# Optimization experiments

Hardware: AMD Instinct MI355X
Metric: run time of the kernel (lower is better)

## Reference

```python
import jax, jax.numpy as jnp
import numpy as np

M_USERS = 100000
N_ITEMS = 50000
NUM_NODES = M_USERS + N_ITEMS
DIM = 64
N_EDGES = 3200000
BATCH = 1024
N_NEGS = 40
REG = 1e-4
NUM_LAYERS = 2


def setup_inputs() -> dict:
    key = jax.random.key(0)
    ks = jax.random.split(key, 14)
    xav = lambda k, shp: jax.random.normal(k, shp, dtype=jnp.float32) * np.float32(np.sqrt(2.0 / (shp[0] + shp[-1])))
    return {
        "E": xav(ks[0], (NUM_NODES, DIM)),
        "E2": xav(ks[1], (NUM_NODES, DIM)),
        "W0": xav(ks[2], (DIM, DIM)),
        "b0": jnp.zeros((DIM,), jnp.float32),
        "W1": xav(ks[3], (DIM, DIM)),
        "b1": jnp.zeros((DIM,), jnp.float32),
        "attn_W": xav(ks[4], (DIM, DIM)),
        "attn_b": jnp.zeros((DIM,), jnp.float32),
        "q_W": xav(ks[5], (1, DIM)),
        "w": jax.random.normal(ks[6], (BATCH,), dtype=jnp.float32),
        "edge_index": jax.random.randint(ks[7], (2, N_EDGES), 0, NUM_NODES, dtype=jnp.int64),
        "u": jax.random.randint(ks[8], (BATCH,), 0, M_USERS, dtype=jnp.int64),
        "v": jax.random.randint(ks[9], (BATCH,), 0, NUM_NODES, dtype=jnp.int64),
        "n": jax.random.randint(ks[10], (BATCH, N_NEGS), 0, NUM_NODES, dtype=jnp.int64),
    }


def _aggregate(E, E2, W0, b0, W1, b1, attn_W, attn_b, q_W, row, col):
    # LightGCN branch: symmetric degree-normalized scatter-add, NUM_LAYERS hops
    deg = jax.ops.segment_sum(jnp.ones_like(col, dtype=E.dtype), col, num_segments=NUM_NODES)
    dinv = jnp.where(deg > 0, jax.lax.rsqrt(jnp.maximum(deg, 1e-12)), 0.0)
    norm = dinv[row] * dinv[col]  # [E]

    def conv(x):
        msg = norm[:, None] * x[row]  # [E, D]
        return jax.ops.segment_sum(msg, col, num_segments=NUM_NODES)

    acc = E
    x = E
    for _ in range(NUM_LAYERS):
        x = conv(x)
        acc = acc + x
    z_p = acc / (NUM_LAYERS + 1)

    # MLP branch (eval mode: dropout disabled)
    h = jax.nn.relu(E2 @ W0.T + b0)
    z_n = jax.nn.relu(h @ W1.T + b1)

    # attention fusion
    w_p = jnp.tanh(z_p @ attn_W.T + attn_b) @ q_W.T  # [NUM_NODES, 1]
    w_n = jnp.tanh(z_n @ attn_W.T + attn_b) @ q_W.T
    alpha = jax.nn.softmax(jnp.concatenate([w_p, w_n], axis=1), axis=1)
    return alpha[:, :1] * z_p + alpha[:, 1:] * z_n


def reference(E, E2, W0, b0, W1, b1, attn_W, attn_b, q_W, w, edge_index, u, v, n):
    row, col = edge_index[0], edge_index[1]
    Z = _aggregate(E, E2, W0, b0, W1, b1, attn_W, attn_b, q_W, row, col)
    u_ = Z[u]            # [B, D]
    v_ = Z[v]            # [B, D]
    n_ = Z[n]            # [B, K, D]
    pos = jnp.sum(u_ * v_, axis=1)                      # [B]
    neg = jnp.einsum('bd,bkd->bk', u_, n_)              # [B, K]
    coef = -0.5 * jnp.sign(w) + 1.5                     # [B]
    sbpr = jax.nn.log_sigmoid(coef[:, None] * pos[:, None] - neg)  # [B, K]
    reg_loss = jnp.sum(u_ ** 2) + jnp.sum(v_ ** 2) + jnp.sum(n_ ** 2)
    return -jnp.sum(sbpr) + REG * reg_loss
```

## Files before the change

### kernel.cpp

```cpp
#include <hip/hip_runtime.h>
#include <hip/hip_fp8.h>
#include <math.h>

#define NUM_NODES 150000
#define DIM 64
#define N_EDGES 3200000
#define BATCH 1024
#define N_NEGS 40
#define REG_COEF 1e-4f

#define BK_BITS 9
#define BK_NODES 512
#define NBK ((NUM_NODES + BK_NODES - 1) >> BK_BITS)
#define TILE 8192
#define NT ((N_EDGES + TILE - 1) / TILE)
#define HSIZE (NBK * NT)
#define SCAN_B 1024
#define NB2 ((HSIZE + SCAN_B - 1) / SCAN_B)
#define NB3 ((NUM_NODES + SCAN_B - 1) / SCAN_B)
#define NLIST (BATCH * (N_NEGS + 2))

typedef _Float16 half2v __attribute__((ext_vector_type(2)));
typedef _Float16 half4v __attribute__((ext_vector_type(4)));

__global__ __launch_bounds__(256) void histo_kernel(const int* __restrict__ col,
                                                    int* __restrict__ hist) {
    __shared__ int h[NBK];
    int t = threadIdx.x;
    for (int i = t; i < NBK; i += 256) h[i] = 0;
    __syncthreads();
    int e0 = blockIdx.x * TILE;
    int e1 = e0 + TILE; if (e1 > N_EDGES) e1 = N_EDGES;
    for (int i = e0 + t; i < e1; i += 256) atomicAdd(&h[col[i] >> BK_BITS], 1);
    __syncthreads();
    for (int i = t; i < NBK; i += 256) hist[i * NT + blockIdx.x] = h[i];
}

__global__ void scan_partial_kernel(const int* __restrict__ src, int* __restrict__ partial, int n) {
    int t = threadIdx.x;
    int g = blockIdx.x * SCAN_B + t;
    int v = (g < n) ? src[g] : 0;
    for (int m = 1; m < 64; m <<= 1) v += __shfl_xor(v, m);
    __shared__ int ws[16];
    if ((t & 63) == 0) ws[t >> 6] = v;
    __syncthreads();
    if (t < 16) {
        int s = ws[t];
        for (int m = 1; m < 16; m <<= 1) s += __shfl_xor(s, m);
        if (t == 0) partial[blockIdx.x] = s;
    }
}

__global__ void scan_base_kernel(int* __restrict__ partial, int nb, int chunks) {
    int l = threadIdx.x;
    int carry = 0;
    for (int c = 0; c < chunks; c++) {
        int idx = c * 64 + l;
        int v = (idx < nb) ? partial[idx] : 0;
        int inc = v;
        for (int m = 1; m < 64; m <<= 1) {
            int t = __shfl_up(inc, m);
            if (l >= m) inc += t;
        }
        int excl = inc - v + carry;
        if (idx < nb) partial[idx] = excl;
        carry += __shfl(inc, 63);
    }
}

__global__ void scan_apply_kernel(int* __restrict__ data, const int* __restrict__ partial, int n) {
    __shared__ int lds[SCAN_B];
    int t = threadIdx.x;
    int g = blockIdx.x * SCAN_B + t;
    int v = (g < n) ? data[g] : 0;
    int val = v;
    lds[t] = val;
    __syncthreads();
    for (int o = 1; o < SCAN_B; o <<= 1) {
        int add = (t >= o) ? lds[t - o] : 0;
        __syncthreads();
        val += add;
        lds[t] = val;
        __syncthreads();
    }
    if (g < n) data[g] = partial[blockIdx.x] + val - v;
}

__global__ void scan_apply2_kernel(const int* __restrict__ src, int* __restrict__ dst,
                                   const int* __restrict__ partial, int n) {
    __shared__ int lds[SCAN_B];
    int t = threadIdx.x;
    int g = blockIdx.x * SCAN_B + t;
    int v = (g < n) ? src[g] : 0;
    int val = v;
    lds[t] = val;
    __syncthreads();
    for (int o = 1; o < SCAN_B; o <<= 1) {
        int add = (t >= o) ? lds[t - o] : 0;
        __syncthreads();
        val += add;
        lds[t] = val;
        __syncthreads();
    }
    if (g < n) dst[g] = partial[blockIdx.x] + val - v;
}

__global__ __launch_bounds__(256) void partition_kernel(const int* __restrict__ row,
                                                        const int* __restrict__ col,
                                                        const int* __restrict__ hist,
                                                        unsigned* __restrict__ staging) {
    __shared__ int base[NBK];
    __shared__ int cnt[NBK];
    int t = threadIdx.x;
    for (int i = t; i < NBK; i += 256) { base[i] = hist[i * NT + blockIdx.x]; cnt[i] = 0; }
    __syncthreads();
    int e0 = blockIdx.x * TILE;
    int e1 = e0 + TILE; if (e1 > N_EDGES) e1 = N_EDGES;
    for (int i = e0 + t; i < e1; i += 256) {
        int c = col[i];
        int b = c >> BK_BITS;
        int r = atomicAdd(&cnt[b], 1);
        staging[base[b] + r] = ((unsigned)(c & (BK_NODES - 1)) << 18) | (unsigned)row[i];
    }
}

__global__ __launch_bounds__(512) void fill3_kernel(const int* __restrict__ hist,
                                                    const unsigned* __restrict__ staging,
                                                    const float* __restrict__ E,
                                                    int* __restrict__ off,
                                                    float* __restrict__ dinv,
                                                    float* __restrict__ sq,
                                                    int* __restrict__ csr_row,
                                                    __hip_fp8x4_e4m3* __restrict__ xnE4) {
    __shared__ int cnt[BK_NODES];
    __shared__ int lds[BK_NODES];
    __shared__ float sdinv[BK_NODES];
    int b = blockIdx.x;
    int t = threadIdx.x;
    int node0 = b << BK_BITS;
    int bstart = hist[b * NT];
    int bend = (b + 1 < NBK) ? hist[(b + 1) * NT] : N_EDGES;
    cnt[t] = 0;
    __syncthreads();
    for (int i = bstart + t; i < bend; i += 512) atomicAdd(&cnt[staging[i] >> 18], 1);
    __syncthreads();
    int v = cnt[t];
    int val = v;
    lds[t] = val;
    __syncthreads();
    for (int o = 1; o < BK_NODES; o <<= 1) {
        int add = (t >= o) ? lds[t - o] : 0;
        __syncthreads();
        val += add;
        lds[t] = val;
        __syncthreads();
    }
    int cursor = bstart + val - v;
    int node = node0 + t;
    float dv = (v > 0) ? rsqrtf((float)v) : 0.f;
    if (node < NUM_NODES) {
        off[node] = cursor;
        dinv[node] = dv;
        sq[node] = sqrtf((float)v);
    }
    sdinv[t] = dv;
    cnt[t] = cursor;
    __syncthreads();
    for (int i = bstart + t; i < bend; i += 512) {
        unsigned s = staging[i];
        int pos = atomicAdd(&cnt[s >> 18], 1);
        csr_row[pos] = (int)(s & 0x3FFFFu);
    }
    int nvalid = NUM_NODES - node0; if (nvalid > BK_NODES) nvalid = BK_NODES;
    int groups = nvalid << 4;
    const float4* E4 = (const float4*)E + ((size_t)node0 << 4);
    __hip_fp8x4_e4m3* out4 = xnE4 + ((size_t)node0 << 4);
    for (int gi = t; gi < groups; gi += 512) {
        float4 e = E4[gi];
        float s = 16.f * sdinv[gi >> 4];
        out4[gi] = __hip_fp8x4_e4m3(make_float4(s * e.x, s * e.y, s * e.z, s * e.w));
    }
    if (b == 0 && t == 0) off[NUM_NODES] = N_EDGES;
}

__global__ void flag_kernel(const int* __restrict__ u, const int* __restrict__ v,
                            const int* __restrict__ n, int* __restrict__ flags) {
    int i = blockIdx.x * blockDim.x + threadIdx.x;
    if (i >= NLIST) return;
    int id;
    if (i < BATCH) id = u[i];
    else if (i < 2 * BATCH) id = v[i - BATCH];
    else id = n[i - 2 * BATCH];
    flags[id] = 1;
}

__global__ void emit_list_kernel(const int* __restrict__ flags, const int* __restrict__ posb,
                                 int* __restrict__ list, int* __restrict__ count) {
    int i = blockIdx.x * blockDim.x + threadIdx.x;
    if (i >= NUM_NODES) return;
    if (flags[i]) list[posb[i]] = i;
    if (i == NUM_NODES - 1) *count = posb[i] + flags[i];
}

__global__ __launch_bounds__(256) void conv1_kernel(const int* __restrict__ off,
                                                    const int* __restrict__ csr_row,
                                                    const float* __restrict__ dinv,
                                                    const __hip_fp8x4_e4m3* __restrict__ xq,
                                                    _Float16* __restrict__ yh) {
    int gid = blockIdx.x * blockDim.x + threadIdx.x;
    int grp = gid >> 4;
    int g = threadIdx.x & 15;
    if (grp >= NUM_NODES) return;
    int start = off[grp];
    int end = off[grp + 1];
    float a0 = 0.f, a1 = 0.f, a2 = 0.f, a3 = 0.f;
    int i = start;
    for (; i + 3 < end; i += 4) {
        int r0 = csr_row[i];
        int r1 = csr_row[i + 1];
        int r2 = csr_row[i + 2];
        int r3 = csr_row[i + 3];
        float4 v0 = static_cast<float4>(xq[((size_t)r0 << 4) + g]);
        float4 v1 = static_cast<float4>(xq[((size_t)r1 << 4) + g]);
        float4 v2 = static_cast<float4>(xq[((size_t)r2 << 4) + g]);
        float4 v3 = static_cast<float4>(xq[((size_t)r3 << 4) + g]);
        a0 += v0.x + v1.x + v2.x + v3.x;
        a1 += v0.y + v1.y + v2.y + v3.y;
        a2 += v0.z + v1.z + v2.z + v3.z;
        a3 += v0.w + v1.w + v2.w + v3.w;
    }
    for (; i < end; ++i) {
        int r = csr_row[i];
        float4 v = static_cast<float4>(xq[((size_t)r << 4) + g]);
        a0 += v.x; a1 += v.y; a2 += v.z; a3 += v.w;
    }
    float dv = dinv[grp];
    float s = dv * dv * (1.f / 16.f);
    union { _Float16 h[4]; short4 s4; } u;
    u.h[0] = (_Float16)(s * a0);
    u.h[1] = (_Float16)(s * a1);
    u.h[2] = (_Float16)(s * a2);
    u.h[3] = (_Float16)(s * a3);
    ((short4*)yh)[((size_t)grp << 4) + g] = u.s4;
}

__global__ __launch_bounds__(256) void conv2_kernel(const int* __restrict__ off,
                                                    const int* __restrict__ csr_row,
                                                    const float* __restrict__ dinv,
                                                    const _Float16* __restrict__ xh,
                                                    float* __restrict__ x2,
                                                    const int* __restrict__ list,
                                                    const int* __restrict__ count) {
    int gid = blockIdx.x * blockDim.x + threadIdx.x;
    int li = gid >> 4;
    int g = threadIdx.x & 15;
    if (li >= *count) return;
    int nd = list[li];
    int start = off[nd];
    int end = off[nd + 1];
    const short4* xh4 = (const short4*)xh;
    float a0 = 0.f, a1 = 0.f, a2 = 0.f, a3 = 0.f;
    int i = start;
    for (; i + 3 < end; i += 4) {
        int r0 = csr_row[i];
        int r1 = csr_row[i + 1];
        int r2 = csr_row[i + 2];
        int r3 = csr_row[i + 3];
        union { short4 s4; _Float16 h[4]; } u0, u1, u2, u3;
        u0.s4 = xh4[((size_t)r0 << 4) + g];
        u1.s4 = xh4[((size_t)r1 << 4) + g];
        u2.s4 = xh4[((size_t)r2 << 4) + g];
        u3.s4 = xh4[((size_t)r3 << 4) + g];
        a0 += (float)u0.h[0] + (float)u1.h[0] + (float)u2.h[0] + (float)u3.h[0];
        a1 += (float)u0.h[1] + (float)u1.h[1] + (float)u2.h[1] + (float)u3.h[1];
        a2 += (float)u0.h[2] + (float)u1.h[2] + (float)u2.h[2] + (float)u3.h[2];
        a3 += (float)u0.h[3] + (float)u1.h[3] + (float)u2.h[3] + (float)u3.h[3];
    }
    for (; i < end; ++i) {
        int r = csr_row[i];
        union { short4 s4; _Float16 h[4]; } u;
        u.s4 = xh4[((size_t)r << 4) + g];
        a0 += (float)u.h[0]; a1 += (float)u.h[1];
        a2 += (float)u.h[2]; a3 += (float)u.h[3];
    }
    float dv = dinv[nd];
    ((float4*)x2)[((size_t)nd << 4) + g] = make_float4(dv * a0, dv * a1, dv * a2, dv * a3);
}

__global__ __launch_bounds__(256, 4) void fuse_kernel(
    const float* __restrict__ E, const float* __restrict__ E2,
    const float* __restrict__ W0, const float* __restrict__ b0,
    const float* __restrict__ W1, const float* __restrict__ b1,
    const float* __restrict__ AW, const float* __restrict__ ab,
    const float* __restrict__ qW,
    const _Float16* __restrict__ xn1, const float* __restrict__ sq,
    const float* x2, float* Z,
    const int* __restrict__ list, const int* __restrict__ count) {
    __shared__ __align__(16) _Float16 W0h[4096];
    __shared__ __align__(16) _Float16 W1h[4096];
    __shared__ __align__(16) _Float16 AWh[4096];
    __shared__ float bb0[64], bb1[64], bab[64], qb[64];
    __shared__ __align__(16) _Float16 xb[4][64];
    __shared__ __align__(16) _Float16 hb[4][64];
    __shared__ __align__(16) _Float16 zpb[4][64];
    __shared__ __align__(16) _Float16 znb[4][64];

    int t = threadIdx.x;
    for (int idx = t; idx < 4096; idx += 256) {
        int j = idx >> 6, k = idx & 63;
        int dst = (k >> 2) * 256 + j * 4 + (k & 3);
        W0h[dst] = (_Float16)W0[idx];
        W1h[dst] = (_Float16)W1[idx];
        AWh[dst] = (_Float16)AW[idx];
    }
    if (t < 64) { bb0[t] = b0[t]; bb1[t] = b1[t]; bab[t] = ab[t]; qb[t] = qW[t]; }
    __syncthreads();

    const int lane = t & 63, w = t >> 6;
    const int cnt = *count;
    const int stride = gridDim.x * 4;
    int li = blockIdx.x * 4 + w;
    if (li >= cnt) return;

    int ndA = list[li];
    {
    }
    size_t bA0 = ((size_t)ndA << 6) + lane;
    float eA = E[bA0], e2A = E2[bA0], x2A = x2[bA0], sqA = sq[ndA];
    _Float16 xnA = xn1[bA0];

    for (; li < cnt; li += stride) {
        int liB = li + stride; liB = (liB < cnt) ? liB : (cnt - 1);
        int ndB = list[liB];
        size_t bB = ((size_t)ndB << 6) + lane;
        float eB = E[bB], e2B = E2[bB], x2B = x2[bB], sqB = sq[ndB];
        _Float16 xnB = xn1[bB];

        size_t base = ((size_t)ndA << 6) + lane;
        float x1v = sqA * (float)xnA;
        float zp = (eA + x1v + x2A) * (1.f / 3.f);
        zpb[w][lane] = (_Float16)zp;
        xb[w][lane] = (_Float16)e2A;
        __builtin_amdgcn_wave_barrier();

        float s0 = bb0[lane], s1 = 0.f;
#pragma unroll
        for (int k4 = 0; k4 < 16; k4++) {
            half4v w4 = *(const half4v*)&W0h[k4 * 256 + lane * 4];
            half4v x4 = *(const half4v*)&xb[w][k4 * 4];
            s0 = __builtin_amdgcn_fdot2((half2v){w4.x, w4.y}, (half2v){x4.x, x4.y}, s0, false);
            s1 = __builtin_amdgcn_fdot2((half2v){w4.z, w4.w}, (half2v){x4.z, x4.w}, s1, false);
        }
        float h = fmaxf(s0 + s1, 0.f);
        hb[w][lane] = (_Float16)h;
        __builtin_amdgcn_wave_barrier();

        s0 = bb1[lane]; s1 = 0.f;
#pragma unroll
        for (int k4 = 0; k4 < 16; k4++) {
            half4v w4 = *(const half4v*)&W1h[k4 * 256 + lane * 4];
            half4v x4 = *(const half4v*)&hb[w][k4 * 4];
            s0 = __builtin_amdgcn_fdot2((half2v){w4.x, w4.y}, (half2v){x4.x, x4.y}, s0, false);
            s1 = __builtin_amdgcn_fdot2((half2v){w4.z, w4.w}, (half2v){x4.z, x4.w}, s1, false);
        }
        float zn = fmaxf(s0 + s1, 0.f);
        znb[w][lane] = (_Float16)zn;
        __builtin_amdgcn_wave_barrier();

        float sp0 = bab[lane], sp1 = 0.f, sn0 = 0.f, sn1 = 0.f;
#pragma unroll
        for (int k4 = 0; k4 < 16; k4++) {
            half4v w4 = *(const half4v*)&AWh[k4 * 256 + lane * 4];
            half4v p4 = *(const half4v*)&zpb[w][k4 * 4];
            half4v n4 = *(const half4v*)&znb[w][k4 * 4];
            sp0 = __builtin_amdgcn_fdot2((half2v){w4.x, w4.y}, (half2v){p4.x, p4.y}, sp0, false);
            sp1 = __builtin_amdgcn_fdot2((half2v){w4.z, w4.w}, (half2v){p4.z, p4.w}, sp1, false);
            sn0 = __builtin_amdgcn_fdot2((half2v){w4.x, w4.y}, (half2v){n4.x, n4.y}, sn0, false);
            sn1 = __builtin_amdgcn_fdot2((half2v){w4.z, w4.w}, (half2v){n4.z, n4.w}, sn1, false);
        }
        float tp = tanhf(sp0 + sp1) * qb[lane];
        float tn = tanhf(bab[lane] + sn0 + sn1) * qb[lane];
        for (int m = 1; m < 64; m <<= 1) {
            tp += __shfl_xor(tp, m);
            tn += __shfl_xor(tn, m);
        }
        float mx = fmaxf(tp, tn);
        float ep = expf(tp - mx), en = expf(tn - mx);
        float inv = 1.f / (ep + en);
        Z[base] = (ep * zp + en * zn) * inv;
        __builtin_amdgcn_wave_barrier();

        ndA = ndB; eA = eB; e2A = e2B; xnA = xnB; x2A = x2B; sqA = sqB;
    }
}

__global__ __launch_bounds__(256) void loss_kernel(const float* __restrict__ Z,
                                                   const float* __restrict__ wv,
                                                   const int* __restrict__ u,
                                                   const int* __restrict__ v,
                                                   const int* __restrict__ n,
                                                   float* __restrict__ out) {
    int wid = (blockIdx.x * blockDim.x + threadIdx.x) >> 6;
    int lane = threadIdx.x & 63;
    if (wid >= BATCH) return;
    float uu = Z[(size_t)u[wid] * DIM + lane];
    float vv = Z[(size_t)v[wid] * DIM + lane];
    float pos = uu * vv;
    for (int m = 1; m < 64; m <<= 1) pos += __shfl_xor(pos, m);
    float reg = uu * uu + vv * vv;
    float wval = wv[wid];
    float sgn = (wval > 0.f ? 1.f : 0.f) - (wval < 0.f ? 1.f : 0.f);
    float coef = -0.5f * sgn + 1.5f;
    float cp = coef * pos;
    float sb = 0.f;
    for (int k = 0; k < N_NEGS; k++) {
        int nid = n[wid * N_NEGS + k];
        float nn = Z[(size_t)nid * DIM + lane];
        float d = uu * nn;
        for (int m = 1; m < 64; m <<= 1) d += __shfl_xor(d, m);
        reg += nn * nn;
        float x = cp - d;
        float ls = (x >= 0.f) ? -log1pf(expf(-x)) : (x - log1pf(expf(x)));
        sb += ls;
    }
    for (int m = 1; m < 64; m <<= 1) reg += __shfl_xor(reg, m);
    if (lane == 0) atomicAdd(out, -sb + REG_COEF * reg);
}

extern "C" void kernel_launch(void* const* d_in, const int* in_sizes, int n_in,
                              void* d_out, int out_size, void* d_ws, size_t ws_size,
                              hipStream_t stream) {
    const float* E  = (const float*)d_in[0];
    const float* E2 = (const float*)d_in[1];
    const float* W0 = (const float*)d_in[2];
    const float* b0 = (const float*)d_in[3];
    const float* W1 = (const float*)d_in[4];
    const float* b1 = (const float*)d_in[5];
    const float* AW = (const float*)d_in[6];
    const float* ab = (const float*)d_in[7];
    const float* qW = (const float*)d_in[8];
    const float* wv = (const float*)d_in[9];
    const int* ei   = (const int*)d_in[10];
    const int* uu   = (const int*)d_in[11];
    const int* vv   = (const int*)d_in[12];
    const int* nn   = (const int*)d_in[13];
    const int* row = ei;
    const int* col = ei + N_EDGES;

    char* ws = (char*)d_ws;
    size_t p = 0;
    auto align_up = [](size_t x) { return (x + 255) & ~(size_t)255; };
    int* off        = (int*)(ws + p); p = align_up(p + (size_t)(NUM_NODES + 1) * 4);
    float* dinv     = (float*)(ws + p); p = align_up(p + (size_t)NUM_NODES * 4);
    float* sq       = (float*)(ws + p); p = align_up(p + (size_t)NUM_NODES * 4);
    int* hist       = (int*)(ws + p); p = align_up(p + (size_t)HSIZE * 4);
    int* partial    = (int*)(ws + p); p = align_up(p + (size_t)NB2 * 4);
    int* csr_row    = (int*)(ws + p); p = align_up(p + (size_t)N_EDGES * 4);
    int* flagi      = (int*)(ws + p); p = align_up(p + (size_t)NUM_NODES * 4);
    int* posb       = (int*)(ws + p); p = align_up(p + (size_t)NUM_NODES * 4);
    int* list       = (int*)(ws + p); p = align_up(p + (size_t)NLIST * 4);
    int* count      = (int*)(ws + p); p = align_up(p + 4);
    __hip_fp8x4_e4m3* xnE4 = (__hip_fp8x4_e4m3*)(ws + p); p = align_up(p + (size_t)NUM_NODES * DIM);
    _Float16* xn1   = (_Float16*)(ws + p); p = align_up(p + (size_t)NUM_NODES * DIM * 2);
    float* x2f      = (float*)(ws + p); p = align_up(p + (size_t)NUM_NODES * DIM * 4);
    float* Z = x2f;
    unsigned* staging = (unsigned*)x2f;

    hipMemsetAsync(d_out, 0, sizeof(float), stream);
    hipMemsetAsync(flagi, 0, (size_t)NUM_NODES * 4, stream);

    histo_kernel<<<NT, 256, 0, stream>>>(col, hist);
    scan_partial_kernel<<<NB2, SCAN_B, 0, stream>>>(hist, partial, HSIZE);
    scan_base_kernel<<<1, 64, 0, stream>>>(partial, NB2, 2);
    scan_apply_kernel<<<NB2, SCAN_B, 0, stream>>>(hist, partial, HSIZE);
    partition_kernel<<<NT, 256, 0, stream>>>(row, col, hist, staging);
    fill3_kernel<<<NBK, 512, 0, stream>>>(hist, staging, E, off, dinv, sq, csr_row, xnE4);

    flag_kernel<<<(NLIST + 255) / 256, 256, 0, stream>>>(uu, vv, nn, flagi);
    scan_partial_kernel<<<NB3, SCAN_B, 0, stream>>>(flagi, partial, NUM_NODES);
    scan_base_kernel<<<1, 64, 0, stream>>>(partial, NB3, 3);
    scan_apply2_kernel<<<NB3, SCAN_B, 0, stream>>>(flagi, posb, partial, NUM_NODES);
    emit_list_kernel<<<(NUM_NODES + 255) / 256, 256, 0, stream>>>(flagi, posb, list, count);

    conv1_kernel<<<(NUM_NODES * 16 + 255) / 256, 256, 0, stream>>>(off, csr_row, dinv, xnE4, xn1);
    conv2_kernel<<<(NLIST * 16 + 255) / 256, 256, 0, stream>>>(off, csr_row, dinv, xn1, x2f, list, count);

    fuse_kernel<<<1280, 256, 0, stream>>>(E, E2, W0, b0, W1, b1, AW, ab, qW,
                                          xn1, sq, x2f, Z, list, count);

    loss_kernel<<<BATCH * 64 / 256, 256, 0, stream>>>(Z, wv, uu, vv, nn, (float*)d_out);
}
```

Measured before the change: 270.5 us.

## Keep fuse weights in registers, process four nodes per wave, unroll conv1 by eight

The fuse kernel now holds each lane's rows of W0, W1 and attn_W as fp16 pairs in registers instead of staging them in shared memory. Each wave now handles a chunk of four nodes per iteration, so every weight register is reused across four dot products and the next chunk's inputs are prefetched. This raises register pressure, so occupancy is lowered to launch_bounds(256,2). Separately, conv1's gather loop is unrolled from four to eight edges to keep more independent loads in flight.

```diff
diff --git a/kernel.cpp b/kernel.cpp
--- a/kernel.cpp
+++ b/kernel.cpp
@@ -215,19 +215,17 @@
     int end = off[grp + 1];
     float a0 = 0.f, a1 = 0.f, a2 = 0.f, a3 = 0.f;
     int i = start;
-    for (; i + 3 < end; i += 4) {
-        int r0 = csr_row[i];
-        int r1 = csr_row[i + 1];
-        int r2 = csr_row[i + 2];
-        int r3 = csr_row[i + 3];
-        float4 v0 = static_cast<float4>(xq[((size_t)r0 << 4) + g]);
-        float4 v1 = static_cast<float4>(xq[((size_t)r1 << 4) + g]);
-        float4 v2 = static_cast<float4>(xq[((size_t)r2 << 4) + g]);
-        float4 v3 = static_cast<float4>(xq[((size_t)r3 << 4) + g]);
-        a0 += v0.x + v1.x + v2.x + v3.x;
-        a1 += v0.y + v1.y + v2.y + v3.y;
-        a2 += v0.z + v1.z + v2.z + v3.z;
-        a3 += v0.w + v1.w + v2.w + v3.w;
+    for (; i + 7 < end; i += 8) {
+        int r[8];
+#pragma unroll
+        for (int k = 0; k < 8; k++) r[k] = csr_row[i + k];
+        float4 v[8];
+#pragma unroll
+        for (int k = 0; k < 8; k++) v[k] = static_cast<float4>(xq[((size_t)r[k] << 4) + g]);
+#pragma unroll
+        for (int k = 0; k < 8; k++) {
+            a0 += v[k].x; a1 += v[k].y; a2 += v[k].z; a3 += v[k].w;
+        }
     }
     for (; i < end; ++i) {
         int r = csr_row[i];
@@ -287,7 +285,7 @@
     ((float4*)x2)[((size_t)nd << 4) + g] = make_float4(dv * a0, dv * a1, dv * a2, dv * a3);
 }
 
-__global__ __launch_bounds__(256, 4) void fuse_kernel(
+__global__ __launch_bounds__(256, 2) void fuse_kernel(
     const float* __restrict__ E, const float* __restrict__ E2,
     const float* __restrict__ W0, const float* __restrict__ b0,
     const float* __restrict__ W1, const float* __restrict__ b1,
@@ -296,101 +294,136 @@
     const _Float16* __restrict__ xn1, const float* __restrict__ sq,
     const float* x2, float* Z,
     const int* __restrict__ list, const int* __restrict__ count) {
-    __shared__ __align__(16) _Float16 W0h[4096];
-    __shared__ __align__(16) _Float16 W1h[4096];
-    __shared__ __align__(16) _Float16 AWh[4096];
-    __shared__ float bb0[64], bb1[64], bab[64], qb[64];
-    __shared__ __align__(16) _Float16 xb[4][64];
-    __shared__ __align__(16) _Float16 hb[4][64];
-    __shared__ __align__(16) _Float16 zpb[4][64];
-    __shared__ __align__(16) _Float16 znb[4][64];
-
-    int t = threadIdx.x;
-    for (int idx = t; idx < 4096; idx += 256) {
-        int j = idx >> 6, k = idx & 63;
-        int dst = (k >> 2) * 256 + j * 4 + (k & 3);
-        W0h[dst] = (_Float16)W0[idx];
-        W1h[dst] = (_Float16)W1[idx];
-        AWh[dst] = (_Float16)AW[idx];
-    }
-    if (t < 64) { bb0[t] = b0[t]; bb1[t] = b1[t]; bab[t] = ab[t]; qb[t] = qW[t]; }
-    __syncthreads();
-
+    const int t = threadIdx.x;
     const int lane = t & 63, w = t >> 6;
+
+    half2v w0r[32], w1r[32], awr[32];
+    {
+        const float4* W0v = (const float4*)(W0 + lane * 64);
+        const float4* W1v = (const float4*)(W1 + lane * 64);
+        const float4* AWv = (const float4*)(AW + lane * 64);
+#pragma unroll
+        for (int k = 0; k < 16; k++) {
+            float4 a = W0v[k];
+            w0r[2 * k] = (half2v){(_Float16)a.x, (_Float16)a.y};
+            w0r[2 * k + 1] = (half2v){(_Float16)a.z, (_Float16)a.w};
+            float4 b = W1v[k];
+            w1r[2 * k] = (half2v){(_Float16)b.x, (_Float16)b.y};
+            w1r[2 * k + 1] = (half2v){(_Float16)b.z, (_Float16)b.w};
+            float4 c = AWv[k];
+            awr[2 * k] = (half2v){(_Float16)c.x, (_Float16)c.y};
+            awr[2 * k + 1] = (half2v){(_Float16)c.z, (_Float16)c.w};
+        }
+    }
+    const float bb0 = b0[lane], bb1 = b1[lane], bab = ab[lane], qb = qW[lane];
+
+    __shared__ __align__(16) _Float16 xb[4][4][64];
+    __shared__ __align__(16) _Float16 zpb[4][4][64];
+    __shared__ __align__(16) _Float16 hb[4][4][64];
+    __shared__ __align__(16) _Float16 znb[4][4][64];
+
     const int cnt = *count;
-    const int stride = gridDim.x * 4;
-    int li = blockIdx.x * 4 + w;
-    if (li >= cnt) return;
-
-    int ndA = list[li];
-    {
-    }
-    size_t bA0 = ((size_t)ndA << 6) + lane;
-    float eA = E[bA0], e2A = E2[bA0], x2A = x2[bA0], sqA = sq[ndA];
-    _Float16 xnA = xn1[bA0];
-
-    for (; li < cnt; li += stride) {
-        int liB = li + stride; liB = (liB < cnt) ? liB : (cnt - 1);
-        int ndB = list[liB];
-        size_t bB = ((size_t)ndB << 6) + lane;
-        float eB = E[bB], e2B = E2[bB], x2B = x2[bB], sqB = sq[ndB];
-        _Float16 xnB = xn1[bB];
-
-        size_t base = ((size_t)ndA << 6) + lane;
-        float x1v = sqA * (float)xnA;
-        float zp = (eA + x1v + x2A) * (1.f / 3.f);
-        zpb[w][lane] = (_Float16)zp;
-        xb[w][lane] = (_Float16)e2A;
+    const int nchunk = (cnt + 3) >> 2;
+    const int cstride = gridDim.x * 4;
+    int ch = blockIdx.x * 4 + w;
+    if (ch >= nchunk) return;
+
+    int ndA[4]; float eA[4], e2A[4], x2A[4], sqA[4]; _Float16 xnA[4];
+#pragma unroll
+    for (int c = 0; c < 4; c++) {
+        int li = ch * 4 + c; li = (li < cnt) ? li : (cnt - 1);
+        int nd = list[li]; ndA[c] = nd;
+        size_t b = ((size_t)nd << 6) + lane;
+        eA[c] = E[b]; e2A[c] = E2[b]; xnA[c] = xn1[b]; x2A[c] = x2[b]; sqA[c] = sq[nd];
+    }
+
+    for (; ch < nchunk; ch += cstride) {
+        int chB = ch + cstride; chB = (chB < nchunk) ? chB : ch;
+        int ndB[4]; float eB[4], e2B[4], x2B[4], sqB[4]; _Float16 xnB[4];
+#pragma unroll
+        for (int c = 0; c < 4; c++) {
+            int li = chB * 4 + c; li = (li < cnt) ? li : (cnt - 1);
+            int nd = list[li]; ndB[c] = nd;
+            size_t b = ((size_t)nd << 6) + lane;
+            eB[c] = E[b]; e2B[c] = E2[b]; xnB[c] = xn1[b]; x2B[c] = x2[b]; sqB[c] = sq[nd];
+        }
+
+        float zp[4];
+#pragma unroll
+        for (int c = 0; c < 4; c++) {
+            zp[c] = (eA[c] + sqA[c] * (float)xnA[c] + x2A[c]) * (1.f / 3.f);
+            zpb[w][c][lane] = (_Float16)zp[c];
+            xb[w][c][lane] = (_Float16)e2A[c];
+        }
         __builtin_amdgcn_wave_barrier();
 
-        float s0 = bb0[lane], s1 = 0.f;
-#pragma unroll
-        for (int k4 = 0; k4 < 16; k4++) {
-            half4v w4 = *(const half4v*)&W0h[k4 * 256 + lane * 4];
-            half4v x4 = *(const half4v*)&xb[w][k4 * 4];
-            s0 = __builtin_amdgcn_fdot2((half2v){w4.x, w4.y}, (half2v){x4.x, x4.y}, s0, false);
-            s1 = __builtin_amdgcn_fdot2((half2v){w4.z, w4.w}, (half2v){x4.z, x4.w}, s1, false);
-        }
-        float h = fmaxf(s0 + s1, 0.f);
-        hb[w][lane] = (_Float16)h;
+        float h[4] = {bb0, bb0, bb0, bb0};
+#pragma unroll
+        for (int k = 0; k < 16; k++) {
+#pragma unroll
+            for (int c = 0; c < 4; c++) {
+                half4v x4 = *(const half4v*)&xb[w][c][k * 4];
+                h[c] = __builtin_amdgcn_fdot2(w0r[2 * k], (half2v){x4.x, x4.y}, h[c], false);
+                h[c] = __builtin_amdgcn_fdot2(w0r[2 * k + 1], (half2v){x4.z, x4.w}, h[c], false);
+            }
+        }
+#pragma unroll
+        for (int c = 0; c < 4; c++) hb[w][c][lane] = (_Float16)fmaxf(h[c], 0.f);
         __builtin_amdgcn_wave_barrier();
 
-        s0 = bb1[lane]; s1 = 0.f;
-#pragma unroll
-        for (int k4 = 0; k4 < 16; k4++) {
-            half4v w4 = *(const half4v*)&W1h[k4 * 256 + lane * 4];
-            half4v x4 = *(const half4v*)&hb[w][k4 * 4];
-            s0 = __builtin_amdgcn_fdot2((half2v){w4.x, w4.y}, (half2v){x4.x, x4.y}, s0, false);
-            s1 = __builtin_amdgcn_fdot2((half2v){w4.z, w4.w}, (half2v){x4.z, x4.w}, s1, false);
-        }
-        float zn = fmaxf(s0 + s1, 0.f);
-        znb[w][lane] = (_Float16)zn;
+        float zn[4] = {bb1, bb1, bb1, bb1};
+#pragma unroll
+        for (int k = 0; k < 16; k++) {
+#pragma unroll
+            for (int c = 0; c < 4; c++) {
+                half4v x4 = *(const half4v*)&hb[w][c][k * 4];
+                zn[c] = __builtin_amdgcn_fdot2(w1r[2 * k], (half2v){x4.x, x4.y}, zn[c], false);
+                zn[c] = __builtin_amdgcn_fdot2(w1r[2 * k + 1], (half2v){x4.z, x4.w}, zn[c], false);
+            }
+        }
+        float znv[4];
+#pragma unroll
+        for (int c = 0; c < 4; c++) {
+            znv[c] = fmaxf(zn[c], 0.f);
+            znb[w][c][lane] = (_Float16)znv[c];
+        }
         __builtin_amdgcn_wave_barrier();
 
-        float sp0 = bab[lane], sp1 = 0.f, sn0 = 0.f, sn1 = 0.f;
-#pragma unroll
-        for (int k4 = 0; k4 < 16; k4++) {
-            half4v w4 = *(const half4v*)&AWh[k4 * 256 + lane * 4];
-            half4v p4 = *(const half4v*)&zpb[w][k4 * 4];
-            half4v n4 = *(const half4v*)&znb[w][k4 * 4];
-            sp0 = __builtin_amdgcn_fdot2((half2v){w4.x, w4.y}, (half2v){p4.x, p4.y}, sp0, false);
-            sp1 = __builtin_amdgcn_fdot2((half2v){w4.z, w4.w}, (half2v){p4.z, p4.w}, sp1, false);
-            sn0 = __builtin_amdgcn_fdot2((half2v){w4.x, w4.y}, (half2v){n4.x, n4.y}, sn0, false);
-            sn1 = __builtin_amdgcn_fdot2((half2v){w4.z, w4.w}, (half2v){n4.z, n4.w}, sn1, false);
-        }
-        float tp = tanhf(sp0 + sp1) * qb[lane];
-        float tn = tanhf(bab[lane] + sn0 + sn1) * qb[lane];
-        for (int m = 1; m < 64; m <<= 1) {
-            tp += __shfl_xor(tp, m);
-            tn += __shfl_xor(tn, m);
-        }
-        float mx = fmaxf(tp, tn);
-        float ep = expf(tp - mx), en = expf(tn - mx);
-        float inv = 1.f / (ep + en);
-        Z[base] = (ep * zp + en * zn) * inv;
+        float sp[4] = {bab, bab, bab, bab}, sn[4] = {bab, bab, bab, bab};
+#pragma unroll
+        for (int k = 0; k < 16; k++) {
+#pragma unroll
+            for (int c = 0; c < 4; c++) {
+                half4v p4 = *(const half4v*)&zpb[w][c][k * 4];
+                half4v n4 = *(const half4v*)&znb[w][c][k * 4];
+                sp[c] = __builtin_amdgcn_fdot2(awr[2 * k], (half2v){p4.x, p4.y}, sp[c], false);
+                sp[c] = __builtin_amdgcn_fdot2(awr[2 * k + 1], (half2v){p4.z, p4.w}, sp[c], false);
+                sn[c] = __builtin_amdgcn_fdot2(awr[2 * k], (half2v){n4.x, n4.y}, sn[c], false);
+                sn[c] = __builtin_amdgcn_fdot2(awr[2 * k + 1], (half2v){n4.z, n4.w}, sn[c], false);
+            }
+        }
+
+#pragma unroll
+        for (int c = 0; c < 4; c++) {
+            float tp = tanhf(sp[c]) * qb;
+            float tn = tanhf(sn[c]) * qb;
+            for (int m = 1; m < 64; m <<= 1) {
+                tp += __shfl_xor(tp, m);
+                tn += __shfl_xor(tn, m);
+            }
+            float mx = fmaxf(tp, tn);
+            float ep = expf(tp - mx), en = expf(tn - mx);
+            float inv = 1.f / (ep + en);
+            if (ch * 4 + c < cnt)
+                Z[((size_t)ndA[c] << 6) + lane] = (ep * zp[c] + en * znv[c]) * inv;
+        }
         __builtin_amdgcn_wave_barrier();
 
-        ndA = ndB; eA = eB; e2A = e2B; xnA = xnB; x2A = x2B; sqA = sqB;
+#pragma unroll
+        for (int c = 0; c < 4; c++) {
+            ndA[c] = ndB[c]; eA[c] = eB[c]; e2A[c] = e2B[c];
+            xnA[c] = xnB[c]; x2A[c] = x2B[c]; sqA[c] = sqB[c];
+        }
     }
 }
 
```

After: 424.2 us. +56.9%, slower.
